# Kernel optimization log

Hardware: AMD Instinct MI355X
Metric: run time of the kernel (lower is better)

Reference implementation:

```python
import jax, jax.numpy as jnp
import numpy as np

EMB = 1024
NHEAD = 16
DILATIONS = (1, 4, 8, 16)
KSIZE = 7
ROT_DIM = 32  # RotaryEmbedding(dim=32): only first 32 channels of each head rotated


def neighbor_idx(T, k, d):
    # NATTEN-style 1D dilated neighborhood: window of k positions on the
    # dilation lattice (same residue class mod d), centered and clamped at borders.
    i = jnp.arange(T)
    r = i % d                      # residue class
    p = i // d                     # position within class
    Lr = (T - r + d - 1) // d      # class length
    s = jnp.clip(p - k // 2, 0, Lr - k)
    j = jnp.arange(k)
    return r[:, None] + (s[:, None] + j[None, :]) * d  # [T, k] int indices


def rope(x, rot_dim=ROT_DIM):
    # lucidrains RotaryEmbedding.rotate_queries_or_keys: interleaved pairs,
    # applied over seq dim (-2), only first rot_dim channels.
    T = x.shape[-2]
    inv = 1.0 / (10000.0 ** (jnp.arange(0, rot_dim, 2, dtype=jnp.float32) / rot_dim))
    freqs = jnp.arange(T, dtype=jnp.float32)[:, None] * inv[None, :]  # [T, rot_dim//2]
    freqs = jnp.repeat(freqs, 2, axis=-1)                             # [T, rot_dim]
    cos, sin = jnp.cos(freqs), jnp.sin(freqs)
    xr, xp = x[..., :rot_dim], x[..., rot_dim:]
    x1, x2 = xr[..., 0::2], xr[..., 1::2]
    rot = jnp.stack([-x2, x1], axis=-1).reshape(xr.shape)
    return jnp.concatenate([xr * cos + rot * sin, xp], axis=-1)


def setup_inputs() -> dict:
    key = jax.random.key(0)
    ks = jax.random.split(key, 5)
    B, T, C = 4, 8192, EMB
    s = 0.02
    return {
        "x": jax.random.normal(ks[0], (B, T, C), jnp.float32),
        "wq": jax.random.normal(ks[1], (C, C), jnp.float32) * s,
        "bq": jnp.zeros((C,), jnp.float32),
        "wk": jax.random.normal(ks[2], (C, C), jnp.float32) * s,
        "bk": jnp.zeros((C,), jnp.float32),
        "wv": jax.random.normal(ks[3], (C, C), jnp.float32) * s,
        "bv": jnp.zeros((C,), jnp.float32),
        "wp": jax.random.normal(ks[4], (C, C), jnp.float32) * s,
        "bp": jnp.zeros((C,), jnp.float32),
    }


def reference(x, wq, bq, wk, bk, wv, bv, wp, bp):
    B, T, C = x.shape
    hs = C // NHEAD

    def heads(w, b):  # torch Linear: x @ W^T + b, then [B, nh, T, hs]
        return (x @ w.T + b).reshape(B, T, NHEAD, hs).transpose(0, 2, 1, 3)

    q, k, v = heads(wq, bq), heads(wk, bk), heads(wv, bv)
    present = jnp.stack([k, v])  # pre-rotary kv cache, as in original

    q, k, v = rope(q), rope(k), rope(v)  # original also rotates v

    gsz = NHEAD // len(DILATIONS)
    outs = []
    for gi, d in enumerate(DILATIONS):
        sl = slice(gi * gsz, (gi + 1) * gsz)
        idx = neighbor_idx(T, KSIZE, d)           # [T, K]
        kk = k[:, sl][:, :, idx]                   # [B, g, T, K, hs]
        vv = v[:, sl][:, :, idx]                   # [B, g, T, K, hs]
        scores = jnp.einsum('bgtd,bgtkd->bgtk', q[:, sl], kk)  # no 1/sqrt(hs), as na1d_qk
        attn = jax.nn.softmax(scores, axis=-1)
        outs.append(jnp.einsum('bgtk,bgtkd->bgtd', attn, vv))
    y = jnp.concatenate(outs, axis=1)              # [B, nh, T, hs]
    y = y.transpose(0, 2, 1, 3).reshape(B, T, C)
    y = y @ wp.T + bp
    return (y, present)
```

## Files before the change

### kernel.cpp

```cpp
#include <hip/hip_runtime.h>

typedef unsigned short ushortT;
typedef unsigned int uint32;
typedef __attribute__((ext_vector_type(8))) short short8;
typedef __attribute__((ext_vector_type(4))) float f32x4;

__device__ __forceinline__ ushortT f2bf(float f) {
    uint32 u = __float_as_uint(f);
    uint32 r = (u + 0x7fffu + ((u >> 16) & 1u)) >> 16;
    return (ushortT)r;
}
__device__ __forceinline__ float bf2f(uint32 v) {
    return __uint_as_float(v << 16);
}

__device__ __forceinline__ void unpack8(uint4 v, float* f) {
    f[0] = bf2f(v.x & 0xffffu); f[1] = bf2f(v.x >> 16);
    f[2] = bf2f(v.y & 0xffffu); f[3] = bf2f(v.y >> 16);
    f[4] = bf2f(v.z & 0xffffu); f[5] = bf2f(v.z >> 16);
    f[6] = bf2f(v.w & 0xffffu); f[7] = bf2f(v.w >> 16);
}

typedef __attribute__((address_space(1))) const void gvoid;
typedef __attribute__((address_space(3))) void lvoid;
__device__ __forceinline__ void gld16(const ushortT* g, ushortT* l) {
    __builtin_amdgcn_global_load_lds((gvoid*)g, (lvoid*)l, 16, 0, 0);
}

__global__ __launch_bounds__(256) void f32_to_bf16_kernel(
    const float* __restrict__ src, ushortT* __restrict__ dst, int n4)
{
    int i = blockIdx.x * 256 + threadIdx.x;
    if (i < n4) {
        float4 v = reinterpret_cast<const float4*>(src)[i];
        ushort4 o;
        o.x = f2bf(v.x); o.y = f2bf(v.y); o.z = f2bf(v.z); o.w = f2bf(v.w);
        reinterpret_cast<ushort4*>(dst)[i] = o;
    }
}

__global__ __launch_bounds__(256) void rope_table_kernel(float2* __restrict__ tab)
{
    int idx = blockIdx.x * 256 + threadIdx.x;
    int t = idx >> 4;
    int i = idx & 15;
    float inv = powf(10000.0f, -(float)i / 16.0f);
    float ang = (float)t * inv;
    tab[idx] = make_float2(cosf(ang), sinf(ang));
}

template<int MODE>
__global__ __launch_bounds__(256) void gemm_kernel(
    const ushortT* __restrict__ A,
    const ushortT* __restrict__ W,
    const float*   __restrict__ bias,
    const float2*  __restrict__ tab,
    ushortT*       __restrict__ Cb,
    float*         __restrict__ Cf,
    int M, int N, int K)
{
    __shared__ ushortT As[128 * 32];
    __shared__ ushortT Bs[128 * 32];
    const int tid  = threadIdx.x;
    const int lane = tid & 63;
    const int wv   = tid >> 6;
    const int wm   = wv >> 1;
    const int wn   = wv & 1;
    const int m0   = blockIdx.y * 128;
    const int n0   = blockIdx.x * 128;

    f32x4 acc[4][4] = {};

    const int r0  = tid >> 2,          cc0 = (tid & 3) * 8;
    const int r1  = (tid + 256) >> 2,  cc1 = ((tid + 256) & 3) * 8;

    const ushortT* Ag0 = A + (size_t)(m0 + r0) * K + cc0;
    const ushortT* Ag1 = A + (size_t)(m0 + r1) * K + cc1;
    const ushortT* Wg0 = W + (size_t)(n0 + r0) * K + cc0;
    const ushortT* Wg1 = W + (size_t)(n0 + r1) * K + cc1;

    ushortT* As0 = As + wv * 512;
    ushortT* As1 = As + 2048 + wv * 512;
    ushortT* Bs0 = Bs + wv * 512;
    ushortT* Bs1 = Bs + 2048 + wv * 512;

    const int kq   = (lane >> 4) * 8;
    const int rsel = lane & 15;

    for (int k0 = 0; k0 < K; k0 += 32) {
        gld16(Ag0 + k0, As0);
        gld16(Ag1 + k0, As1);
        gld16(Wg0 + k0, Bs0);
        gld16(Wg1 + k0, Bs1);
        __syncthreads();

        short8 af[4], bfr[4];
        #pragma unroll
        for (int i = 0; i < 4; ++i) {
            af[i]  = *reinterpret_cast<const short8*>(As + (wm * 64 + i * 16 + rsel) * 32 + kq);
            bfr[i] = *reinterpret_cast<const short8*>(Bs + (wn * 64 + i * 16 + rsel) * 32 + kq);
        }
        #pragma unroll
        for (int i = 0; i < 4; ++i)
            #pragma unroll
            for (int j = 0; j < 4; ++j)
                acc[i][j] = __builtin_amdgcn_mfma_f32_16x16x32_bf16(af[i], bfr[j], acc[i][j], 0, 0, 0);
        __syncthreads();
    }

    #pragma unroll
    for (int j = 0; j < 4; ++j) {
        const int colb = n0 + wn * 64 + j * 16 + rsel;
        const int d    = colb & 63;
        const float bv = bias[colb];
        #pragma unroll
        for (int i = 0; i < 4; ++i) {
            const int rowbase = m0 + wm * 64 + i * 16 + (lane >> 4) * 4;
            #pragma unroll
            for (int e = 0; e < 4; ++e) {
                const int row = rowbase + e;
                const float val = acc[i][j][e] + bv;
                if (MODE == 1) {
                    const int b = row >> 13, t = row & 8191;
                    const int h = colb >> 6;
                    Cf[(((size_t)b * 16 + h) * 8192 + t) * 64 + d] = val;
                }
                if (MODE == 2) {
                    Cf[(size_t)row * N + colb] = val;
                } else {
                    const float pv = __shfl_xor(val, 1, 64);
                    float ov = val;
                    if (d < 32) {
                        const int t = row & 8191;
                        const float2 cs = tab[t * 16 + (d >> 1)];
                        ov = (d & 1) ? fmaf(val, cs.x,  pv * cs.y)
                                     : fmaf(val, cs.x, -pv * cs.y);
                    }
                    Cb[(size_t)row * N + colb] = f2bf(ov);
                }
            }
        }
    }
}

__global__ __launch_bounds__(256) void natt_kernel(
    const ushortT* __restrict__ Q,
    const ushortT* __restrict__ Kl,
    const ushortT* __restrict__ Vl,
    ushortT*       __restrict__ O)
{
    const int T = 8192;
    const int tid  = threadIdx.x;
    const int lane = tid & 63;
    const int tloc = lane >> 3;
    const int c    = lane & 7;

    const int wq   = (blockIdx.x * 256 + tid) >> 6;
    const int qidx = wq * 8 + tloc;
    const int t = qidx & (T - 1);
    const int h = (qidx >> 13) & 15;
    const int b = qidx >> 17;

    const int shifts[4] = {0, 2, 3, 4};
    const int sh = shifts[h >> 2];
    const int dd = 1 << sh;

    const int r  = t & (dd - 1);
    const int p  = t >> sh;
    const int Lr = ((T - 1 - r) >> sh) + 1;
    int s = p - 3;
    const int smax = Lr - 7;
    s = s < 0 ? 0 : (s > smax ? smax : s);
    const int tbase = r + (s << sh);

    const size_t qoff = ((size_t)(b * T + t)) * 1024 + h * 64 + c * 8;
    float qf[8];
    unpack8(*reinterpret_cast<const uint4*>(Q + qoff), qf);

    const size_t cbase = ((size_t)b * T) * 1024 + h * 64 + c * 8;

    float sc[7];
    #pragma unroll
    for (int j = 0; j < 7; ++j) {
        const int tj = tbase + (j << sh);
        float kf[8];
        unpack8(*reinterpret_cast<const uint4*>(Kl + cbase + (size_t)tj * 1024), kf);
        float pp = 0.f;
        #pragma unroll
        for (int i = 0; i < 8; ++i) pp = fmaf(qf[i], kf[i], pp);
        pp += __shfl_xor(pp, 1, 64);
        pp += __shfl_xor(pp, 2, 64);
        pp += __shfl_xor(pp, 4, 64);
        sc[j] = pp;
    }

    float mx = sc[0];
    #pragma unroll
    for (int j = 1; j < 7; ++j) mx = fmaxf(mx, sc[j]);
    float den = 0.f;
    #pragma unroll
    for (int j = 0; j < 7; ++j) { sc[j] = __expf(sc[j] - mx); den += sc[j]; }
    const float inv = 1.0f / den;

    float out[8] = {};
    #pragma unroll
    for (int j = 0; j < 7; ++j) {
        const int tj = tbase + (j << sh);
        float vf[8];
        unpack8(*reinterpret_cast<const uint4*>(Vl + cbase + (size_t)tj * 1024), vf);
        #pragma unroll
        for (int i = 0; i < 8; ++i) out[i] = fmaf(sc[j], vf[i], out[i]);
    }

    short8 ov;
    #pragma unroll
    for (int i = 0; i < 8; ++i) ov[i] = (short)f2bf(out[i] * inv);
    *reinterpret_cast<short8*>(const_cast<ushortT*>(O + qoff)) = ov;
}

extern "C" void kernel_launch(void* const* d_in, const int* in_sizes, int n_in,
                              void* d_out, int out_size, void* d_ws, size_t ws_size,
                              hipStream_t stream)
{
    const float* x  = (const float*)d_in[0];
    const float* wq = (const float*)d_in[1];
    const float* bq = (const float*)d_in[2];
    const float* wk = (const float*)d_in[3];
    const float* bk = (const float*)d_in[4];
    const float* wv = (const float*)d_in[5];
    const float* bv = (const float*)d_in[6];
    const float* wp = (const float*)d_in[7];
    const float* bp = (const float*)d_in[8];

    const int B = 4, T = 8192, C = 1024;
    const int M = B * T;
    const size_t MC = (size_t)M * C;

    char* ws = (char*)d_ws;
    ushortT* xb   = (ushortT*)ws;
    ushortT* wqb  = (ushortT*)(ws + (size_t)64 * 1024 * 1024);
    ushortT* wkb  = wqb + (size_t)C * C;
    ushortT* wvb  = wkb + (size_t)C * C;
    ushortT* wpb  = wvb + (size_t)C * C;
    ushortT* qlin = (ushortT*)(ws + (size_t)72 * 1024 * 1024);
    ushortT* klin = qlin + MC;
    ushortT* vlin = klin + MC;
    float2*  tab  = (float2*)(ws + (size_t)264 * 1024 * 1024);

    float* y     = (float*)d_out;
    float* presK = y + MC;
    float* presV = presK + MC;

    rope_table_kernel<<<512, 256, 0, stream>>>(tab);

    f32_to_bf16_kernel<<<(int)(MC / 4 / 256), 256, 0, stream>>>(x, xb, (int)(MC / 4));
    const int wn4 = C * C / 4;
    f32_to_bf16_kernel<<<(wn4 + 255) / 256, 256, 0, stream>>>(wq, wqb, wn4);
    f32_to_bf16_kernel<<<(wn4 + 255) / 256, 256, 0, stream>>>(wk, wkb, wn4);
    f32_to_bf16_kernel<<<(wn4 + 255) / 256, 256, 0, stream>>>(wv, wvb, wn4);
    f32_to_bf16_kernel<<<(wn4 + 255) / 256, 256, 0, stream>>>(wp, wpb, wn4);

    dim3 gg(C / 128, M / 128);
    gemm_kernel<0><<<gg, 256, 0, stream>>>(xb, wqb, bq, tab, qlin, nullptr, M, C, C);
    gemm_kernel<1><<<gg, 256, 0, stream>>>(xb, wkb, bk, tab, klin, presK, M, C, C);
    gemm_kernel<1><<<gg, 256, 0, stream>>>(xb, wvb, bv, tab, vlin, presV, M, C, C);

    natt_kernel<<<(B * 16 * T) / 32, 256, 0, stream>>>(qlin, klin, vlin, xb);

    gemm_kernel<2><<<gg, 256, 0, stream>>>(xb, wpb, bp, tab, nullptr, y, M, C, C);
}
```

Baseline: 673.7 us.

## Rewrite GEMMs as 256x256-tile, 4-stage pipelined kernels with swizzled LDS

Replaces the 128x128 single-buffered GEMM with a 256x256 tile, 512-thread kernel that uses a 4-deep ring of LDS buffers. Global-to-LDS loads for tile t+3 are issued while the current tile is computed, with explicit vmcnt waits, barriers and setprio around the MFMA bursts. An XOR swizzle on LDS columns is meant to avoid bank conflicts, and block-ID swizzling groups tiles for L2 reuse. The aim is to hide global-memory latency and raise MFMA utilisation. In exchange it needs 128KB of dynamic LDS per block and hand-tuned waitcnt logic that assumes K is divisible and at least 3 tiles.

Result: faster. 623.0 us (-7.5%).

```diff
diff --git a/kernel.cpp b/kernel.cpp
--- a/kernel.cpp
+++ b/kernel.cpp
@@ -49,8 +49,15 @@
     tab[idx] = make_float2(cosf(ang), sinf(ang));
 }
 
+
+__device__ __forceinline__ short8 ldsfrag(const ushortT* region, int row, int g) {
+    int e = (row << 5) + (g << 3);
+    e ^= ((row >> 1) & 3) << 3;
+    return *reinterpret_cast<const short8*>(region + e);
+}
+
 template<int MODE>
-__global__ __launch_bounds__(256) void gemm_kernel(
+__global__ __launch_bounds__(512, 2) void gemm256_kernel(
     const ushortT* __restrict__ A,
     const ushortT* __restrict__ W,
     const float*   __restrict__ bias,
@@ -59,67 +66,111 @@
     float*         __restrict__ Cf,
     int M, int N, int K)
 {
-    __shared__ ushortT As[128 * 32];
-    __shared__ ushortT Bs[128 * 32];
+    extern __shared__ ushortT lds[];
     const int tid  = threadIdx.x;
     const int lane = tid & 63;
     const int wv   = tid >> 6;
-    const int wm   = wv >> 1;
-    const int wn   = wv & 1;
-    const int m0   = blockIdx.y * 128;
-    const int n0   = blockIdx.x * 128;
-
-    f32x4 acc[4][4] = {};
-
-    const int r0  = tid >> 2,          cc0 = (tid & 3) * 8;
-    const int r1  = (tid + 256) >> 2,  cc1 = ((tid + 256) & 3) * 8;
-
-    const ushortT* Ag0 = A + (size_t)(m0 + r0) * K + cc0;
-    const ushortT* Ag1 = A + (size_t)(m0 + r1) * K + cc1;
-    const ushortT* Wg0 = W + (size_t)(n0 + r0) * K + cc0;
-    const ushortT* Wg1 = W + (size_t)(n0 + r1) * K + cc1;
-
-    ushortT* As0 = As + wv * 512;
-    ushortT* As1 = As + 2048 + wv * 512;
-    ushortT* Bs0 = Bs + wv * 512;
-    ushortT* Bs1 = Bs + 2048 + wv * 512;
-
-    const int kq   = (lane >> 4) * 8;
+    const int wm   = wv >> 2;
+    const int wn   = wv & 3;
+    const int g    = lane >> 4;
     const int rsel = lane & 15;
 
-    for (int k0 = 0; k0 < K; k0 += 32) {
-        gld16(Ag0 + k0, As0);
-        gld16(Ag1 + k0, As1);
-        gld16(Wg0 + k0, Bs0);
-        gld16(Wg1 + k0, Bs1);
-        __syncthreads();
-
-        short8 af[4], bfr[4];
-        #pragma unroll
-        for (int i = 0; i < 4; ++i) {
-            af[i]  = *reinterpret_cast<const short8*>(As + (wm * 64 + i * 16 + rsel) * 32 + kq);
-            bfr[i] = *reinterpret_cast<const short8*>(Bs + (wn * 64 + i * 16 + rsel) * 32 + kq);
+    const int bid = blockIdx.x;
+    const int swz = (bid & 7) * 64 + (bid >> 3);
+    const int tm  = swz & 127, tn = swz >> 7;
+    const int m0  = tm * 256,  n0 = tn * 256;
+
+    const int crow = tid >> 2;
+    const int ccol = ((tid & 3) ^ ((tid >> 3) & 3)) * 8;
+    const ushortT* gA0 = A + (size_t)(m0 + crow) * K + ccol;
+    const ushortT* gA1 = gA0 + (size_t)128 * K;
+    const ushortT* gB0 = W + (size_t)(n0 + crow) * K + ccol;
+    const ushortT* gB1 = gB0 + (size_t)128 * K;
+
+    const int dst0 = wv * 512;
+    const int dst1 = 4096 + wv * 512;
+
+    #pragma unroll
+    for (int t = 0; t < 3; ++t) {
+        ushortT* ra = lds + t * 16384;
+        ushortT* rb = ra + 8192;
+        gld16(gA0 + t * 32, ra + dst0);
+        gld16(gA1 + t * 32, ra + dst1);
+        gld16(gB0 + t * 32, rb + dst0);
+        gld16(gB1 + t * 32, rb + dst1);
+    }
+    asm volatile("s_waitcnt vmcnt(8)" ::: "memory");
+    __builtin_amdgcn_s_barrier();
+
+    f32x4 acc[8][4] = {};
+    const int NT = K >> 5;
+
+    #pragma unroll 1
+    for (int t = 0; t < NT; ++t) {
+        const ushortT* ra = lds + (t & 3) * 16384;
+        const ushortT* rb = ra + 8192;
+
+        short8 Bf[4], Af[4];
+        #pragma unroll
+        for (int fn = 0; fn < 4; ++fn) Bf[fn] = ldsfrag(rb, wn * 64 + fn * 16 + rsel, g);
+        #pragma unroll
+        for (int fm = 0; fm < 4; ++fm) Af[fm] = ldsfrag(ra, wm * 128 + fm * 16 + rsel, g);
+        if (t + 3 < NT) {
+            ushortT* wa = lds + ((t + 3) & 3) * 16384;
+            gld16(gA0 + (t + 3) * 32, wa + dst0);
+            gld16(gA1 + (t + 3) * 32, wa + dst1);
         }
-        #pragma unroll
-        for (int i = 0; i < 4; ++i)
+        asm volatile("" ::: "memory");
+        __builtin_amdgcn_s_barrier();
+        asm volatile("s_waitcnt lgkmcnt(0)" ::: "memory");
+        __builtin_amdgcn_sched_barrier(0);
+        __builtin_amdgcn_s_setprio(1);
+        #pragma unroll
+        for (int fm = 0; fm < 4; ++fm)
             #pragma unroll
-            for (int j = 0; j < 4; ++j)
-                acc[i][j] = __builtin_amdgcn_mfma_f32_16x16x32_bf16(af[i], bfr[j], acc[i][j], 0, 0, 0);
-        __syncthreads();
-    }
-
-    #pragma unroll
-    for (int j = 0; j < 4; ++j) {
-        const int colb = n0 + wn * 64 + j * 16 + rsel;
+            for (int fn = 0; fn < 4; ++fn)
+                acc[fm][fn] = __builtin_amdgcn_mfma_f32_16x16x32_bf16(Af[fm], Bf[fn], acc[fm][fn], 0, 0, 0);
+        __builtin_amdgcn_s_setprio(0);
+        asm volatile("" ::: "memory");
+        __builtin_amdgcn_s_barrier();
+
+        #pragma unroll
+        for (int fm = 0; fm < 4; ++fm) Af[fm] = ldsfrag(ra, wm * 128 + 64 + fm * 16 + rsel, g);
+        if (t + 3 < NT) {
+            ushortT* wb = lds + ((t + 3) & 3) * 16384 + 8192;
+            gld16(gB0 + (t + 3) * 32, wb + dst0);
+            gld16(gB1 + (t + 3) * 32, wb + dst1);
+        }
+        if (t < NT - 3)      { asm volatile("s_waitcnt vmcnt(8)" ::: "memory"); }
+        else if (t == NT - 3){ asm volatile("s_waitcnt vmcnt(4)" ::: "memory"); }
+        else if (t == NT - 2){ asm volatile("s_waitcnt vmcnt(0)" ::: "memory"); }
+        asm volatile("" ::: "memory");
+        __builtin_amdgcn_s_barrier();
+        asm volatile("s_waitcnt lgkmcnt(0)" ::: "memory");
+        __builtin_amdgcn_sched_barrier(0);
+        __builtin_amdgcn_s_setprio(1);
+        #pragma unroll
+        for (int fm = 0; fm < 4; ++fm)
+            #pragma unroll
+            for (int fn = 0; fn < 4; ++fn)
+                acc[4 + fm][fn] = __builtin_amdgcn_mfma_f32_16x16x32_bf16(Af[fm], Bf[fn], acc[4 + fm][fn], 0, 0, 0);
+        __builtin_amdgcn_s_setprio(0);
+        asm volatile("" ::: "memory");
+        __builtin_amdgcn_s_barrier();
+    }
+
+    #pragma unroll
+    for (int fn = 0; fn < 4; ++fn) {
+        const int colb = n0 + wn * 64 + fn * 16 + rsel;
         const int d    = colb & 63;
         const float bv = bias[colb];
         #pragma unroll
-        for (int i = 0; i < 4; ++i) {
-            const int rowbase = m0 + wm * 64 + i * 16 + (lane >> 4) * 4;
+        for (int am = 0; am < 8; ++am) {
+            const int rowbase = m0 + wm * 128 + am * 16 + g * 4;
             #pragma unroll
             for (int e = 0; e < 4; ++e) {
                 const int row = rowbase + e;
-                const float val = acc[i][j][e] + bv;
+                const float val = acc[am][fn][e] + bv;
                 if (MODE == 1) {
                     const int b = row >> 13, t = row & 8191;
                     const int h = colb >> 6;
@@ -251,6 +302,13 @@
     float* presK = y + MC;
     float* presV = presK + MC;
 
+    hipFuncSetAttribute((const void*)gemm256_kernel<0>,
+                        hipFuncAttributeMaxDynamicSharedMemorySize, 131072);
+    hipFuncSetAttribute((const void*)gemm256_kernel<1>,
+                        hipFuncAttributeMaxDynamicSharedMemorySize, 131072);
+    hipFuncSetAttribute((const void*)gemm256_kernel<2>,
+                        hipFuncAttributeMaxDynamicSharedMemorySize, 131072);
+
     rope_table_kernel<<<512, 256, 0, stream>>>(tab);
 
     f32_to_bf16_kernel<<<(int)(MC / 4 / 256), 256, 0, stream>>>(x, xb, (int)(MC / 4));
@@ -260,12 +318,12 @@
     f32_to_bf16_kernel<<<(wn4 + 255) / 256, 256, 0, stream>>>(wv, wvb, wn4);
     f32_to_bf16_kernel<<<(wn4 + 255) / 256, 256, 0, stream>>>(wp, wpb, wn4);
 
-    dim3 gg(C / 128, M / 128);
-    gemm_kernel<0><<<gg, 256, 0, stream>>>(xb, wqb, bq, tab, qlin, nullptr, M, C, C);
-    gemm_kernel<1><<<gg, 256, 0, stream>>>(xb, wkb, bk, tab, klin, presK, M, C, C);
-    gemm_kernel<1><<<gg, 256, 0, stream>>>(xb, wvb, bv, tab, vlin, presV, M, C, C);
+    const int nwg = (M / 256) * (C / 256);
+    gemm256_kernel<0><<<nwg, 512, 131072, stream>>>(xb, wqb, bq, tab, qlin, nullptr, M, C, C);
+    gemm256_kernel<1><<<nwg, 512, 131072, stream>>>(xb, wkb, bk, tab, klin, presK, M, C, C);
+    gemm256_kernel<1><<<nwg, 512, 131072, stream>>>(xb, wvb, bv, tab, vlin, presV, M, C, C);
 
     natt_kernel<<<(B * 16 * T) / 32, 256, 0, stream>>>(qlin, klin, vlin, xb);
 
-    gemm_kernel<2><<<gg, 256, 0, stream>>>(xb, wpb, bp, tab, nullptr, y, M, C, C);
-}
+    gemm256_kernel<2><<<nwg, 512, 131072, stream>>>(xb, wpb, bp, tab, nullptr, y, M, C, C);
+}
```
